# Optimization experiments

Hardware: AMD Instinct MI355X
Metric: run time of the kernel (lower is better)

## Reference

```python
import jax, jax.numpy as jnp
import numpy as np

D = 512      # d_model
H = 8        # n_heads
HD = D // H  # head_dim = 64
PS = 4       # patch_size
B, T, P = 4, 4096, 1024


def setup_inputs() -> dict:
    key = jax.random.key(0)
    ks = jax.random.split(key, 12)
    s = 1.0 / np.sqrt(D)
    return {
        "token_hidden": jax.random.normal(ks[0], (B, T, D), jnp.float32),
        "patch_hidden": jax.random.normal(ks[1], (B, P, D), jnp.float32),
        "Wq": jax.random.normal(ks[2], (D, D), jnp.float32) * s,
        "Wk": jax.random.normal(ks[3], (D, D), jnp.float32) * s,
        "Wv": jax.random.normal(ks[4], (D, D), jnp.float32) * s,
        "bq": jax.random.normal(ks[5], (D,), jnp.float32) * 0.02,
        "bk": jax.random.normal(ks[6], (D,), jnp.float32) * 0.02,
        "bv": jax.random.normal(ks[7], (D,), jnp.float32) * 0.02,
        "Wo": jax.random.normal(ks[8], (D, D), jnp.float32) * s,
        "bo": jax.random.normal(ks[9], (D,), jnp.float32) * 0.02,
    }


def reference(token_hidden, patch_hidden, Wq, Wk, Wv, bq, bk, bv, Wo, bo):
    b, t, _ = token_hidden.shape
    p = patch_hidden.shape[1]
    # QKV projections (equivalent to nn.MultiheadAttention in_proj)
    q = (token_hidden @ Wq + bq).reshape(b, t, H, HD)
    k = (patch_hidden @ Wk + bk).reshape(b, p, H, HD)
    v = (patch_hidden @ Wv + bv).reshape(b, p, H, HD)
    # scaled dot-product scores: [b, h, t, p]
    scores = jnp.einsum('bthd,bphd->bhtp', q, k) / jnp.sqrt(jnp.asarray(HD, q.dtype))
    # block-causal token-to-patch mask: token i attends to patches 0..i//PS
    allowed = jnp.arange(p)[None, :] <= (jnp.arange(t)[:, None] // PS)  # [t, p]
    scores = jnp.where(allowed[None, None, :, :], scores, -jnp.inf)
    attn = jax.nn.softmax(scores, axis=-1)
    ctx = jnp.einsum('bhtp,bphd->bthd', attn, v).reshape(b, t, D)
    out = ctx @ Wo + bo  # out_proj
    return token_hidden + out
```

## Files before the change

### kernel.cpp

```cpp
#include <hip/hip_runtime.h>
#include <stdint.h>

#define DM 512
#define NH 8
#define HDIM 64
#define TT 4096
#define PP 1024

typedef float f32x4 __attribute__((ext_vector_type(4)));
typedef __bf16 bf16x8 __attribute__((ext_vector_type(8)));
typedef __bf16 bf16x4 __attribute__((ext_vector_type(4)));
typedef unsigned short u16x8 __attribute__((ext_vector_type(8)));
typedef unsigned short u16x4 __attribute__((ext_vector_type(4)));
typedef unsigned int u32x2 __attribute__((ext_vector_type(2)));
typedef unsigned int u32x4 __attribute__((ext_vector_type(4)));

static __device__ __forceinline__ unsigned short f2bf(float f) {
  unsigned u = __builtin_bit_cast(unsigned, f);
  u += 0x7fff + ((u >> 16) & 1);
  return (unsigned short)(u >> 16);
}

static __device__ __forceinline__ unsigned packtr(float a, float b) {
  return __builtin_amdgcn_perm(__builtin_bit_cast(unsigned, b),
                               __builtin_bit_cast(unsigned, a), 0x07060302u);
}

static __device__ __forceinline__ float fexp2(float x) {
#if __has_builtin(__builtin_amdgcn_exp2f)
  return __builtin_amdgcn_exp2f(x);
#else
  return __expf(x * 0.69314718055994531f);
#endif
}

static __device__ __forceinline__ void load_lds16(const void* g, void* l) {
  __builtin_amdgcn_global_load_lds(
      (__attribute__((address_space(1))) void*)g,
      (__attribute__((address_space(3))) void*)l, 16, 0, 0);
}

static __device__ __forceinline__ f32x4 mfma16(bf16x8 a, bf16x8 b, f32x4 c) {
  return __builtin_amdgcn_mfma_f32_16x16x32_bf16(a, b, c, 0, 0, 0);
}

static __device__ __forceinline__ bf16x8 p_exchange(unsigned w0, unsigned w1,
                                                    unsigned w2, unsigned w3,
                                                    int q, int c) {
#if __has_builtin(__builtin_amdgcn_permlane32_swap) && \
    __has_builtin(__builtin_amdgcn_permlane16_swap)
  (void)q; (void)c;
  auto s02 = __builtin_amdgcn_permlane32_swap(w0, w2, false, false);
  auto t02 = __builtin_amdgcn_permlane16_swap(s02[0], s02[1], false, false);
  auto s13 = __builtin_amdgcn_permlane32_swap(w1, w3, false, false);
  auto t13 = __builtin_amdgcn_permlane16_swap(s13[0], s13[1], false, false);
  u32x4 pd = {(unsigned)t02[0], (unsigned)t13[0], (unsigned)t02[1], (unsigned)t13[1]};
  return __builtin_bit_cast(bf16x8, pd);
#else
  const int a0 = (c + (q & 1) * 32) * 4;
  const int a2 = (c + 16 + (q & 1) * 32) * 4;
  const bool lo = (q < 2);
  unsigned d0 = lo ? (unsigned)__builtin_amdgcn_ds_bpermute(a0, (int)w0)
                   : (unsigned)__builtin_amdgcn_ds_bpermute(a0, (int)w2);
  unsigned d1 = lo ? (unsigned)__builtin_amdgcn_ds_bpermute(a0, (int)w1)
                   : (unsigned)__builtin_amdgcn_ds_bpermute(a0, (int)w3);
  unsigned d2 = lo ? (unsigned)__builtin_amdgcn_ds_bpermute(a2, (int)w0)
                   : (unsigned)__builtin_amdgcn_ds_bpermute(a2, (int)w2);
  unsigned d3 = lo ? (unsigned)__builtin_amdgcn_ds_bpermute(a2, (int)w1)
                   : (unsigned)__builtin_amdgcn_ds_bpermute(a2, (int)w3);
  u32x4 pd = {d0, d1, d2, d3};
  return __builtin_bit_cast(bf16x8, pd);
#endif
}

static __device__ __forceinline__ int sw_rd(int c, int q) {
  return ((q + (c >> 1)) & 3) * 8;
}

__global__ __launch_bounds__(256) void k_convW(
    const float* __restrict__ wq, const float* __restrict__ wk,
    const float* __restrict__ wv, const float* __restrict__ wo,
    unsigned short* __restrict__ wt) {
  const int wi = blockIdx.x * 256 + threadIdx.x;
  int wid = wi >> 16;
  int e = (wi & 65535) << 2;
  int k = e >> 9, n = e & 511;
  const float* w = (wid == 0) ? wq : (wid == 1) ? wk : (wid == 2) ? wv : wo;
  f32x4 v = *(const f32x4*)&w[e];
  unsigned short* wtb = wt + (wid << 18);
#pragma unroll
  for (int i = 0; i < 4; ++i) wtb[(n + i) * 512 + k] = f2bf(v[i]);
}

template <int MODE>
__device__ __forceinline__ void gemm_qkv_body(
    const float* __restrict__ A, const unsigned short* __restrict__ Wt,
    const float* __restrict__ bias, unsigned short* __restrict__ outb,
    int bid, unsigned short* sA, unsigned short* sB, float scale) {
  const int tid = threadIdx.x;
  const int wave = tid >> 6, lane = tid & 63;
  const int q = lane >> 4, c = lane & 15;
  const int bm = bid >> 2, bn = bid & 3;
  const int wm = (wave >> 1) * 64, wn = (wave & 1) * 64;
  const int lr = lane >> 2, lc = (lane & 3) * 8;
  const int swW = (((lane & 3) + (lane >> 3)) & 3) * 8;
  const int swS = (((lane & 3) - (lane >> 3)) & 3) * 8;

  f32x4 acc[4][4];
#pragma unroll
  for (int i = 0; i < 4; ++i)
#pragma unroll
    for (int j = 0; j < 4; ++j) acc[i][j] = (f32x4){0.f, 0.f, 0.f, 0.f};

  const int rowA0 = bm * 128, rowB0 = bn * 128;

  f32x4 rA0[2][2], rA1[2][2];

  auto a_issue = [&](int t, f32x4 (&r)[2][2]) {
    const int kn = t * 32;
#pragma unroll
    for (int qq = 0; qq < 2; ++qq) {
      const float* src = &A[(rowA0 + (wave * 2 + qq) * 16 + lr) * 512 + kn + lc];
      r[qq][0] = *(const f32x4*)src;
      r[qq][1] = *(const f32x4*)(src + 4);
    }
  };
  auto a_write = [&](int t, f32x4 (&r)[2][2]) {
    unsigned short* dA = sA + (t & 1) * 4096;
#pragma unroll
    for (int qq = 0; qq < 2; ++qq) {
      u16x4 lo = __builtin_bit_cast(u16x4, __builtin_convertvector(r[qq][0], bf16x4));
      u16x4 hi = __builtin_bit_cast(u16x4, __builtin_convertvector(r[qq][1], bf16x4));
      u16x8 o = {lo[0], lo[1], lo[2], lo[3], hi[0], hi[1], hi[2], hi[3]};
      *(u16x8*)&dA[(wave * 2 + qq) * 512 + lr * 32 + swW] = o;
    }
  };
  auto b_issue = [&](int t) {
    const int kn = t * 32;
    unsigned short* dB = sB + (t % 3) * 4096;
#pragma unroll
    for (int qq = 0; qq < 2; ++qq) {
      const int chunk = wave * 2 + qq;
      load_lds16(&Wt[(rowB0 + chunk * 16 + lr) * 512 + kn + swS], &dB[chunk * 512]);
    }
  };

  a_issue(0, rA0);
  b_issue(0);
  a_issue(1, rA1);
  b_issue(1);
  asm volatile("s_waitcnt vmcnt(6)" ::: "memory");
  a_write(0, rA0);
  asm volatile("s_waitcnt lgkmcnt(0)" ::: "memory");
  __builtin_amdgcn_s_barrier();

#pragma unroll 1
  for (int i = 0; i < 16; ++i) {
    const bool ev = ((i & 1) == 0);
    if (i + 2 < 16) {
      if (ev) a_issue(i + 2, rA0);
      else    a_issue(i + 2, rA1);
      b_issue(i + 2);
    }
    const unsigned short* curA = sA + (i & 1) * 4096;
    const unsigned short* curB = sB + (i % 3) * 4096;
    bf16x8 af[4], bfr[4];
#pragma unroll
    for (int mt = 0; mt < 4; ++mt)
      af[mt] = __builtin_bit_cast(bf16x8,
          *(const u16x8*)&curA[(wm + mt * 16 + c) * 32 + sw_rd(c, q)]);
#pragma unroll
    for (int nt = 0; nt < 4; ++nt)
      bfr[nt] = __builtin_bit_cast(bf16x8,
          *(const u16x8*)&curB[(wn + nt * 16 + c) * 32 + sw_rd(c, q)]);
#pragma unroll
    for (int mt = 0; mt < 4; ++mt)
#pragma unroll
      for (int nt = 0; nt < 4; ++nt) {
        if (MODE == 2)
          acc[mt][nt] = mfma16(af[mt], bfr[nt], acc[mt][nt]);
        else
          acc[mt][nt] = mfma16(bfr[nt], af[mt], acc[mt][nt]);
      }
    if (i < 15) {
      if (i < 14) asm volatile("s_waitcnt vmcnt(6)" ::: "memory");
      else        asm volatile("s_waitcnt vmcnt(0)" ::: "memory");
      if (ev) a_write(i + 1, rA1);
      else    a_write(i + 1, rA0);
      asm volatile("s_waitcnt lgkmcnt(0)" ::: "memory");
      __builtin_amdgcn_s_barrier();
    }
  }

  if (MODE == 2) {
#pragma unroll
    for (int nt = 0; nt < 4; ++nt) {
      const int col = bn * 128 + wn + nt * 16 + c;
      const float bcol = bias[col];
#pragma unroll
      for (int mt = 0; mt < 4; ++mt) {
        const int row0 = bm * 128 + wm + mt * 16 + q * 4;
        u16x4 o;
#pragma unroll
        for (int r = 0; r < 4; ++r) o[r] = f2bf(acc[mt][nt][r] + bcol);
        *(u16x4*)&outb[((row0 >> 10) << 19) + (col << 10) + (row0 & 1023)] = o;
      }
    }
  } else {
#pragma unroll
    for (int mt = 0; mt < 4; ++mt) {
      const int row = bm * 128 + wm + mt * 16 + c;
#pragma unroll
      for (int nt = 0; nt < 4; ++nt) {
        const int col0 = bn * 128 + wn + nt * 16 + q * 4;
        const f32x4 bv = *(const f32x4*)&bias[col0];
        u16x4 o;
#pragma unroll
        for (int r = 0; r < 4; ++r) o[r] = f2bf((acc[mt][nt][r] + bv[r]) * scale);
        *(u16x4*)&outb[row * 512 + col0] = o;
      }
    }
  }
}

__global__ __launch_bounds__(256, 3) void k_gemm_qkv(
    const float* __restrict__ tok, const float* __restrict__ pat,
    const unsigned short* __restrict__ WT,
    const float* __restrict__ bq, const float* __restrict__ bk,
    const float* __restrict__ bv,
    unsigned short* __restrict__ QB, unsigned short* __restrict__ KB,
    unsigned short* __restrict__ VTB) {
  __shared__ unsigned short sA[2 * 128 * 32];
  __shared__ unsigned short sB[3 * 128 * 32];
  const int hw = blockIdx.x;
  const int bid = (hw & 7) * 96 + (hw >> 3);
  if (bid < 512) {
    gemm_qkv_body<0>(tok, WT, bq, QB, bid, sA, sB, 0.18033688011112042f);
  } else if (bid < 640) {
    gemm_qkv_body<1>(pat, WT + 262144, bk, KB, bid - 512, sA, sB, 1.0f);
  } else {
    gemm_qkv_body<2>(pat, WT + 524288, bv, VTB, bid - 640, sA, sB, 1.0f);
  }
}

__global__ __launch_bounds__(256) void k_gemm_o(
    const unsigned short* __restrict__ A, const unsigned short* __restrict__ Wt,
    const float* __restrict__ bias, float* __restrict__ outf,
    const float* __restrict__ resid) {
  __shared__ unsigned short sA[3 * 128 * 32];
  __shared__ unsigned short sB[3 * 128 * 32];
  const int tid = threadIdx.x;
  const int wave = tid >> 6, lane = tid & 63;
  const int q = lane >> 4, c = lane & 15;
  const int hw = blockIdx.x;
  const int obid = (hw & 7) * 64 + (hw >> 3);
  const int bm = obid >> 2, bn = obid & 3;
  const int wm = (wave >> 1) * 64, wn = (wave & 1) * 64;
  const int lr = lane >> 2;
  const int swS = (((lane & 3) - (lane >> 3)) & 3) * 8;

  f32x4 acc[4][4];
#pragma unroll
  for (int i = 0; i < 4; ++i)
#pragma unroll
    for (int j = 0; j < 4; ++j) acc[i][j] = (f32x4){0.f, 0.f, 0.f, 0.f};

  const int rowA0 = bm * 128, rowB0 = bn * 128;

  auto stage = [&](int t) {
    const int kn = t * 32;
    unsigned short* dA = sA + (t % 3) * 4096;
    unsigned short* dB = sB + (t % 3) * 4096;
#pragma unroll
    for (int qq = 0; qq < 2; ++qq) {
      const int chunk = wave * 2 + qq;
      load_lds16(&A[(rowA0 + chunk * 16 + lr) * 512 + kn + swS], &dA[chunk * 512]);
      load_lds16(&Wt[(rowB0 + chunk * 16 + lr) * 512 + kn + swS], &dB[chunk * 512]);
    }
  };

  stage(0);
  stage(1);
  asm volatile("s_waitcnt vmcnt(4)" ::: "memory");
  __builtin_amdgcn_s_barrier();

#pragma unroll 1
  for (int i = 0; i < 16; ++i) {
    if (i + 2 < 16) stage(i + 2);
    const unsigned short* curA = sA + (i % 3) * 4096;
    const unsigned short* curB = sB + (i % 3) * 4096;
    bf16x8 af[4], bfr[4];
#pragma unroll
    for (int mt = 0; mt < 4; ++mt)
      af[mt] = __builtin_bit_cast(bf16x8,
          *(const u16x8*)&curA[(wm + mt * 16 + c) * 32 + sw_rd(c, q)]);
#pragma unroll
    for (int nt = 0; nt < 4; ++nt)
      bfr[nt] = __builtin_bit_cast(bf16x8,
          *(const u16x8*)&curB[(wn + nt * 16 + c) * 32 + sw_rd(c, q)]);
#pragma unroll
    for (int mt = 0; mt < 4; ++mt)
#pragma unroll
      for (int nt = 0; nt < 4; ++nt)
        acc[mt][nt] = mfma16(bfr[nt], af[mt], acc[mt][nt]);
    if (i < 15) {
      if (i + 2 < 16) asm volatile("s_waitcnt vmcnt(4)" ::: "memory");
      else            asm volatile("s_waitcnt vmcnt(0)" ::: "memory");
      __builtin_amdgcn_s_barrier();
    }
  }

#pragma unroll
  for (int mt = 0; mt < 4; ++mt) {
    const int row = bm * 128 + wm + mt * 16 + c;
#pragma unroll
    for (int nt = 0; nt < 4; ++nt) {
      const int col0 = bn * 128 + wn + nt * 16 + q * 4;
      const int o = row * 512 + col0;
      const f32x4 bv = *(const f32x4*)&bias[col0];
      const f32x4 rv = *(const f32x4*)&resid[o];
      f32x4 ov;
#pragma unroll
      for (int r = 0; r < 4; ++r) ov[r] = acc[mt][nt][r] + bv[r] + rv[r];
      *(f32x4*)&outf[o] = ov;
    }
  }
}

__global__ __launch_bounds__(256) void k_attn(
    const unsigned short* __restrict__ Q,
    const unsigned short* __restrict__ K,
    const unsigned short* __restrict__ VT,
    unsigned short* __restrict__ CTX) {
  __shared__ unsigned short sK[2][32 * 88];
  __shared__ unsigned short sV[2][64 * 40];

  const int tid = threadIdx.x;
  const int lane = tid & 63;
  const int wave = tid >> 6;
  const int q = lane >> 4, c = lane & 15;

  const int g = blockIdx.x >> 5;
  const int tg = (g < 16) ? g : 47 - g;
  const int bh = blockIdx.x & 31;
  const int b = bh >> 3, h = bh & 7;
  const int t0 = tg * 128 + wave * 32;
  const int tA = t0 + c, tB = t0 + 16 + c;

  const int qbA = (b * TT + tA) * 512 + h * 64 + q * 8;
  const int qbB = (b * TT + tB) * 512 + h * 64 + q * 8;
  const bf16x8 qfA0 = __builtin_bit_cast(bf16x8, *(const u16x8*)&Q[qbA]);
  const bf16x8 qfA1 = __builtin_bit_cast(bf16x8, *(const u16x8*)&Q[qbA + 32]);
  const bf16x8 qfB0 = __builtin_bit_cast(bf16x8, *(const u16x8*)&Q[qbB]);
  const bf16x8 qfB1 = __builtin_bit_cast(bf16x8, *(const u16x8*)&Q[qbB + 32]);

  f32x4 oA[4], oB[4];
#pragma unroll
  for (int m = 0; m < 4; ++m) {
    oA[m] = (f32x4){0.f, 0.f, 0.f, 0.f};
    oB[m] = (f32x4){0.f, 0.f, 0.f, 0.f};
  }
  f32x4 lA = (f32x4){0.f, 0.f, 0.f, 0.f};
  f32x4 lB = lA;
  const u16x8 onesu = {0x3F80, 0x3F80, 0x3F80, 0x3F80, 0x3F80, 0x3F80, 0x3F80, 0x3F80};
  const bf16x8 ones = __builtin_bit_cast(bf16x8, onesu);

  const int ntile = tg + 1;
  const int krow = tid >> 3, kcol = (tid & 7) * 8;
  const int vrow = tid >> 2, vcol = (tid & 3) * 8;
  const int kg = (b * PP + krow) * 512 + h * 64 + kcol;
  const int vg = (b << 19) + ((h * 64 + vrow) << 10) + vcol;

  u16x8 kreg = *(const u16x8*)&K[kg];
  u16x8 vreg = *(const u16x8*)&VT[vg];
  *(u16x8*)&sK[0][krow * 88 + kcol] = kreg;
  *(u16x8*)&sV[0][vrow * 40 + vcol] = vreg;
  __syncthreads();

#pragma unroll 1
  for (int pt = 0; pt < ntile; ++pt) {
    const int buf = pt & 1;
    const bool more = (pt + 1 < ntile);
    if (more) {
      kreg = *(const u16x8*)&K[kg + (pt + 1) * 32 * 512];
      vreg = *(const u16x8*)&VT[vg + (pt + 1) * 32];
    }
    const unsigned short* bK = sK[buf];
    const unsigned short* bV = sV[buf];

    const bf16x8 ka0 = __builtin_bit_cast(bf16x8, *(const u16x8*)&bK[c * 88 + q * 8]);
    const bf16x8 ka1 = __builtin_bit_cast(bf16x8, *(const u16x8*)&bK[c * 88 + 32 + q * 8]);
    const bf16x8 kb0 = __builtin_bit_cast(bf16x8, *(const u16x8*)&bK[(16 + c) * 88 + q * 8]);
    const bf16x8 kb1 = __builtin_bit_cast(bf16x8, *(const u16x8*)&bK[(16 + c) * 88 + 32 + q * 8]);

    const f32x4 z = (f32x4){0.f, 0.f, 0.f, 0.f};
    __builtin_amdgcn_s_setprio(1);
    f32x4 sA0 = mfma16(ka1, qfA1, mfma16(ka0, qfA0, z));
    f32x4 sA1 = mfma16(kb1, qfA1, mfma16(kb0, qfA0, z));
    f32x4 sB0 = mfma16(ka1, qfB1, mfma16(ka0, qfB0, z));
    f32x4 sB1 = mfma16(kb1, qfB1, mfma16(kb0, qfB0, z));
    __builtin_amdgcn_s_setprio(0);

    if (pt + 1 == ntile) {
      const int p0 = pt * 32;
      const int limA = tA >> 2, limB = tB >> 2;
      const int pb0 = p0 + q * 4, pb1 = p0 + 16 + q * 4;
#pragma unroll
      for (int r = 0; r < 4; ++r) {
        if (pb0 + r > limA) sA0[r] = -1e30f;
        if (pb1 + r > limA) sA1[r] = -1e30f;
        if (pb0 + r > limB) sB0[r] = -1e30f;
        if (pb1 + r > limB) sB1[r] = -1e30f;
      }
    }

    float pA0[4], pA1[4], pB0[4], pB1[4];
#pragma unroll
    for (int r = 0; r < 4; ++r) {
      pA0[r] = fexp2(sA0[r]);
      pA1[r] = fexp2(sA1[r]);
      pB0[r] = fexp2(sB0[r]);
      pB1[r] = fexp2(sB1[r]);
    }

    const bf16x8 pbA = p_exchange(packtr(pA0[0], pA0[1]), packtr(pA0[2], pA0[3]),
                                  packtr(pA1[0], pA1[1]), packtr(pA1[2], pA1[3]), q, c);
    const bf16x8 pbB = p_exchange(packtr(pB0[0], pB0[1]), packtr(pB0[2], pB0[3]),
                                  packtr(pB1[0], pB1[1]), packtr(pB1[2], pB1[3]), q, c);

    __builtin_amdgcn_s_setprio(1);
#pragma unroll
    for (int mt = 0; mt < 4; ++mt) {
      const bf16x8 vf =
          __builtin_bit_cast(bf16x8, *(const u16x8*)&bV[(mt * 16 + c) * 40 + q * 8]);
      oA[mt] = mfma16(vf, pbA, oA[mt]);
      oB[mt] = mfma16(vf, pbB, oB[mt]);
    }
    lA = mfma16(ones, pbA, lA);
    lB = mfma16(ones, pbB, lB);
    __builtin_amdgcn_s_setprio(0);

    if (more) {
      *(u16x8*)&sK[buf ^ 1][krow * 88 + kcol] = kreg;
      *(u16x8*)&sV[buf ^ 1][vrow * 40 + vcol] = vreg;
      __syncthreads();
    }
  }

  const float invA = 1.f / lA[0];
  const float invB = 1.f / lB[0];
  const int obA = (b * TT + tA) * 512 + h * 64 + q * 4;
  const int obB = (b * TT + tB) * 512 + h * 64 + q * 4;
#pragma unroll
  for (int mt = 0; mt < 4; ++mt) {
    u16x4 oa, ob;
#pragma unroll
    for (int r = 0; r < 4; ++r) {
      oa[r] = f2bf(oA[mt][r] * invA);
      ob[r] = f2bf(oB[mt][r] * invB);
    }
    *(u16x4*)&CTX[obA + mt * 16] = oa;
    *(u16x4*)&CTX[obB + mt * 16] = ob;
  }
}

extern "C" void kernel_launch(void* const* d_in, const int* in_sizes, int n_in,
                              void* d_out, int out_size, void* d_ws, size_t ws_size,
                              hipStream_t stream) {
  const float* tok = (const float*)d_in[0];
  const float* pat = (const float*)d_in[1];
  const float* Wq = (const float*)d_in[2];
  const float* Wk = (const float*)d_in[3];
  const float* Wv = (const float*)d_in[4];
  const float* bq = (const float*)d_in[5];
  const float* bk = (const float*)d_in[6];
  const float* bv = (const float*)d_in[7];
  const float* Wo = (const float*)d_in[8];
  const float* bo = (const float*)d_in[9];
  float* out = (float*)d_out;

  unsigned short* ws = (unsigned short*)d_ws;
  unsigned short* WT = ws;
  unsigned short* QB = ws + 11534336;
  unsigned short* KB = ws + 19922944;
  unsigned short* VTB = ws + 22020096;
  unsigned short* CTX = ws + 24117248;

  k_convW<<<1024, 256, 0, stream>>>(Wq, Wk, Wv, Wo, WT);
  k_gemm_qkv<<<768, 256, 0, stream>>>(tok, pat, WT, bq, bk, bv, QB, KB, VTB);
  k_attn<<<1024, 256, 0, stream>>>(QB, KB, VTB, CTX);
  k_gemm_o<<<512, 256, 0, stream>>>(CTX, WT + 786432, bo, out, tok);
}
```

Before: 196.0 us.

## Double K-tile depth to 64 in projection GEMMs with 8-way LDS swizzle

```diff
diff --git a/kernel.cpp b/kernel.cpp
--- a/kernel.cpp
+++ b/kernel.cpp
@@ -73,9 +73,6 @@
 #endif
 }
 
-static __device__ __forceinline__ int sw_rd(int c, int q) {
-  return ((q + (c >> 1)) & 3) * 8;
-}
 
 __global__ __launch_bounds__(256) void k_convW(
     const float* __restrict__ wq, const float* __restrict__ wk,
@@ -102,9 +99,9 @@
   const int q = lane >> 4, c = lane & 15;
   const int bm = bid >> 2, bn = bid & 3;
   const int wm = (wave >> 1) * 64, wn = (wave & 1) * 64;
-  const int lr = lane >> 2, lc = (lane & 3) * 8;
-  const int swW = (((lane & 3) + (lane >> 3)) & 3) * 8;
-  const int swS = (((lane & 3) - (lane >> 3)) & 3) * 8;
+  const int ar = tid >> 1, ah = (tid & 1) * 32;
+  const int als = (tid & 1) * 4;
+  const int bg = (((lane & 7) - (lane >> 3)) & 7) * 8;
 
   f32x4 acc[4][4];
 #pragma unroll
@@ -114,80 +111,76 @@
 
   const int rowA0 = bm * 128, rowB0 = bn * 128;
 
-  f32x4 rA0[2][2], rA1[2][2];
-
-  auto a_issue = [&](int t, f32x4 (&r)[2][2]) {
-    const int kn = t * 32;
-#pragma unroll
-    for (int qq = 0; qq < 2; ++qq) {
-      const float* src = &A[(rowA0 + (wave * 2 + qq) * 16 + lr) * 512 + kn + lc];
-      r[qq][0] = *(const f32x4*)src;
-      r[qq][1] = *(const f32x4*)(src + 4);
-    }
+  f32x4 rA[8];
+
+  auto a_issue = [&](int t) {
+    const float* src = &A[(rowA0 + ar) * 512 + t * 64 + ah];
+#pragma unroll
+    for (int j = 0; j < 8; ++j) rA[j] = *(const f32x4*)(src + j * 4);
   };
-  auto a_write = [&](int t, f32x4 (&r)[2][2]) {
-    unsigned short* dA = sA + (t & 1) * 4096;
-#pragma unroll
-    for (int qq = 0; qq < 2; ++qq) {
-      u16x4 lo = __builtin_bit_cast(u16x4, __builtin_convertvector(r[qq][0], bf16x4));
-      u16x4 hi = __builtin_bit_cast(u16x4, __builtin_convertvector(r[qq][1], bf16x4));
+  auto a_write = [&](int t) {
+    unsigned short* dA = sA + (t & 1) * 8192;
+#pragma unroll
+    for (int j = 0; j < 4; ++j) {
+      u16x4 lo = __builtin_bit_cast(u16x4, __builtin_convertvector(rA[2 * j], bf16x4));
+      u16x4 hi = __builtin_bit_cast(u16x4, __builtin_convertvector(rA[2 * j + 1], bf16x4));
       u16x8 o = {lo[0], lo[1], lo[2], lo[3], hi[0], hi[1], hi[2], hi[3]};
-      *(u16x8*)&dA[(wave * 2 + qq) * 512 + lr * 32 + swW] = o;
+      const int phys = ((als + j) + (ar & 7)) & 7;
+      *(u16x8*)&dA[ar * 64 + phys * 8] = o;
     }
   };
   auto b_issue = [&](int t) {
-    const int kn = t * 32;
-    unsigned short* dB = sB + (t % 3) * 4096;
-#pragma unroll
-    for (int qq = 0; qq < 2; ++qq) {
-      const int chunk = wave * 2 + qq;
-      load_lds16(&Wt[(rowB0 + chunk * 16 + lr) * 512 + kn + swS], &dB[chunk * 512]);
+    unsigned short* dB = sB + (t & 1) * 8192;
+#pragma unroll
+    for (int ch = 0; ch < 4; ++ch) {
+      const int r0 = wave * 32 + ch * 8;
+      load_lds16(&Wt[(rowB0 + r0 + (lane >> 3)) * 512 + t * 64 + bg],
+                 &dB[r0 * 64]);
     }
   };
 
-  a_issue(0, rA0);
+  a_issue(0);
   b_issue(0);
-  a_issue(1, rA1);
-  b_issue(1);
-  asm volatile("s_waitcnt vmcnt(6)" ::: "memory");
-  a_write(0, rA0);
-  asm volatile("s_waitcnt lgkmcnt(0)" ::: "memory");
+  asm volatile("s_waitcnt vmcnt(4)" ::: "memory");
+  a_write(0);
+  asm volatile("s_waitcnt vmcnt(0) lgkmcnt(0)" ::: "memory");
   __builtin_amdgcn_s_barrier();
 
 #pragma unroll 1
-  for (int i = 0; i < 16; ++i) {
-    const bool ev = ((i & 1) == 0);
-    if (i + 2 < 16) {
-      if (ev) a_issue(i + 2, rA0);
-      else    a_issue(i + 2, rA1);
-      b_issue(i + 2);
-    }
-    const unsigned short* curA = sA + (i & 1) * 4096;
-    const unsigned short* curB = sB + (i % 3) * 4096;
-    bf16x8 af[4], bfr[4];
-#pragma unroll
-    for (int mt = 0; mt < 4; ++mt)
-      af[mt] = __builtin_bit_cast(bf16x8,
-          *(const u16x8*)&curA[(wm + mt * 16 + c) * 32 + sw_rd(c, q)]);
-#pragma unroll
-    for (int nt = 0; nt < 4; ++nt)
-      bfr[nt] = __builtin_bit_cast(bf16x8,
-          *(const u16x8*)&curB[(wn + nt * 16 + c) * 32 + sw_rd(c, q)]);
-#pragma unroll
-    for (int mt = 0; mt < 4; ++mt)
-#pragma unroll
-      for (int nt = 0; nt < 4; ++nt) {
-        if (MODE == 2)
-          acc[mt][nt] = mfma16(af[mt], bfr[nt], acc[mt][nt]);
-        else
-          acc[mt][nt] = mfma16(bfr[nt], af[mt], acc[mt][nt]);
-      }
-    if (i < 15) {
-      if (i < 14) asm volatile("s_waitcnt vmcnt(6)" ::: "memory");
-      else        asm volatile("s_waitcnt vmcnt(0)" ::: "memory");
-      if (ev) a_write(i + 1, rA1);
-      else    a_write(i + 1, rA0);
-      asm volatile("s_waitcnt lgkmcnt(0)" ::: "memory");
+  for (int i = 0; i < 8; ++i) {
+    const bool more = (i + 1 < 8);
+    if (more) {
+      a_issue(i + 1);
+      b_issue(i + 1);
+    }
+    const unsigned short* curA = sA + (i & 1) * 8192;
+    const unsigned short* curB = sB + (i & 1) * 8192;
+#pragma unroll
+    for (int ks = 0; ks < 2; ++ks) {
+      const int ph = ((ks * 4 + q + (c & 7)) & 7) * 8;
+      bf16x8 af[4], bfr[4];
+#pragma unroll
+      for (int mt = 0; mt < 4; ++mt)
+        af[mt] = __builtin_bit_cast(bf16x8,
+            *(const u16x8*)&curA[(wm + mt * 16 + c) * 64 + ph]);
+#pragma unroll
+      for (int nt = 0; nt < 4; ++nt)
+        bfr[nt] = __builtin_bit_cast(bf16x8,
+            *(const u16x8*)&curB[(wn + nt * 16 + c) * 64 + ph]);
+#pragma unroll
+      for (int mt = 0; mt < 4; ++mt)
+#pragma unroll
+        for (int nt = 0; nt < 4; ++nt) {
+          if (MODE == 2)
+            acc[mt][nt] = mfma16(af[mt], bfr[nt], acc[mt][nt]);
+          else
+            acc[mt][nt] = mfma16(bfr[nt], af[mt], acc[mt][nt]);
+        }
+    }
+    if (more) {
+      asm volatile("s_waitcnt vmcnt(4)" ::: "memory");
+      a_write(i + 1);
+      asm volatile("s_waitcnt vmcnt(0) lgkmcnt(0)" ::: "memory");
       __builtin_amdgcn_s_barrier();
     }
   }
@@ -223,15 +216,15 @@
   }
 }
 
-__global__ __launch_bounds__(256, 3) void k_gemm_qkv(
+__global__ __launch_bounds__(256, 2) void k_gemm_qkv(
     const float* __restrict__ tok, const float* __restrict__ pat,
     const unsigned short* __restrict__ WT,
     const float* __restrict__ bq, const float* __restrict__ bk,
     const float* __restrict__ bv,
     unsigned short* __restrict__ QB, unsigned short* __restrict__ KB,
     unsigned short* __restrict__ VTB) {
-  __shared__ unsigned short sA[2 * 128 * 32];
-  __shared__ unsigned short sB[3 * 128 * 32];
+  __shared__ unsigned short sA[2 * 128 * 64];
+  __shared__ unsigned short sB[2 * 128 * 64];
   const int hw = blockIdx.x;
   const int bid = (hw & 7) * 96 + (hw >> 3);
   if (bid < 512) {
@@ -243,12 +236,12 @@
   }
 }
 
-__global__ __launch_bounds__(256) void k_gemm_o(
+__global__ __launch_bounds__(256, 2) void k_gemm_o(
     const unsigned short* __restrict__ A, const unsigned short* __restrict__ Wt,
     const float* __restrict__ bias, float* __restrict__ outf,
     const float* __restrict__ resid) {
-  __shared__ unsigned short sA[3 * 128 * 32];
-  __shared__ unsigned short sB[3 * 128 * 32];
+  __shared__ unsigned short sA[2 * 128 * 64];
+  __shared__ unsigned short sB[2 * 128 * 64];
   const int tid = threadIdx.x;
   const int wave = tid >> 6, lane = tid & 63;
   const int q = lane >> 4, c = lane & 15;
@@ -256,8 +249,7 @@
   const int obid = (hw & 7) * 64 + (hw >> 3);
   const int bm = obid >> 2, bn = obid & 3;
   const int wm = (wave >> 1) * 64, wn = (wave & 1) * 64;
-  const int lr = lane >> 2;
-  const int swS = (((lane & 3) - (lane >> 3)) & 3) * 8;
+  const int bg = (((lane & 7) - (lane >> 3)) & 7) * 8;
 
   f32x4 acc[4][4];
 #pragma unroll
@@ -268,44 +260,47 @@
   const int rowA0 = bm * 128, rowB0 = bn * 128;
 
   auto stage = [&](int t) {
-    const int kn = t * 32;
-    unsigned short* dA = sA + (t % 3) * 4096;
-    unsigned short* dB = sB + (t % 3) * 4096;
-#pragma unroll
-    for (int qq = 0; qq < 2; ++qq) {
-      const int chunk = wave * 2 + qq;
-      load_lds16(&A[(rowA0 + chunk * 16 + lr) * 512 + kn + swS], &dA[chunk * 512]);
-      load_lds16(&Wt[(rowB0 + chunk * 16 + lr) * 512 + kn + swS], &dB[chunk * 512]);
+    unsigned short* dA = sA + (t & 1) * 8192;
+    unsigned short* dB = sB + (t & 1) * 8192;
+#pragma unroll
+    for (int ch = 0; ch < 4; ++ch) {
+      const int r0 = wave * 32 + ch * 8;
+      const int rsrc = r0 + (lane >> 3);
+      load_lds16(&A[(rowA0 + rsrc) * 512 + t * 64 + bg], &dA[r0 * 64]);
+      load_lds16(&Wt[(rowB0 + rsrc) * 512 + t * 64 + bg], &dB[r0 * 64]);
     }
   };
 
   stage(0);
-  stage(1);
-  asm volatile("s_waitcnt vmcnt(4)" ::: "memory");
+  asm volatile("s_waitcnt vmcnt(0)" ::: "memory");
   __builtin_amdgcn_s_barrier();
 
 #pragma unroll 1
-  for (int i = 0; i < 16; ++i) {
-    if (i + 2 < 16) stage(i + 2);
-    const unsigned short* curA = sA + (i % 3) * 4096;
-    const unsigned short* curB = sB + (i % 3) * 4096;
-    bf16x8 af[4], bfr[4];
-#pragma unroll
-    for (int mt = 0; mt < 4; ++mt)
-      af[mt] = __builtin_bit_cast(bf16x8,
-          *(const u16x8*)&curA[(wm + mt * 16 + c) * 32 + sw_rd(c, q)]);
-#pragma unroll
-    for (int nt = 0; nt < 4; ++nt)
-      bfr[nt] = __builtin_bit_cast(bf16x8,
-          *(const u16x8*)&curB[(wn + nt * 16 + c) * 32 + sw_rd(c, q)]);
-#pragma unroll
-    for (int mt = 0; mt < 4; ++mt)
+  for (int i = 0; i < 8; ++i) {
+    const bool more = (i + 1 < 8);
+    if (more) stage(i + 1);
+    const unsigned short* curA = sA + (i & 1) * 8192;
+    const unsigned short* curB = sB + (i & 1) * 8192;
+#pragma unroll
+    for (int ks = 0; ks < 2; ++ks) {
+      const int ph = ((ks * 4 + q + (c & 7)) & 7) * 8;
+      bf16x8 af[4], bfr[4];
+#pragma unroll
+      for (int mt = 0; mt < 4; ++mt)
+        af[mt] = __builtin_bit_cast(bf16x8,
+            *(const u16x8*)&curA[(wm + mt * 16 + c) * 64 + ph]);
 #pragma unroll
       for (int nt = 0; nt < 4; ++nt)
-        acc[mt][nt] = mfma16(bfr[nt], af[mt], acc[mt][nt]);
-    if (i < 15) {
-      if (i + 2 < 16) asm volatile("s_waitcnt vmcnt(4)" ::: "memory");
-      else            asm volatile("s_waitcnt vmcnt(0)" ::: "memory");
+        bfr[nt] = __builtin_bit_cast(bf16x8,
+            *(const u16x8*)&curB[(wn + nt * 16 + c) * 64 + ph]);
+#pragma unroll
+      for (int mt = 0; mt < 4; ++mt)
+#pragma unroll
+        for (int nt = 0; nt < 4; ++nt)
+          acc[mt][nt] = mfma16(bfr[nt], af[mt], acc[mt][nt]);
+    }
+    if (more) {
+      asm volatile("s_waitcnt vmcnt(0)" ::: "memory");
       __builtin_amdgcn_s_barrier();
     }
   }
```

Result: slower. 205.0 us (+4.6%).

## Load GEMM A operand directly into MFMA registers, bypassing LDS staging

Applied to the files above, without the earlier changes.

```diff
diff --git a/kernel.cpp b/kernel.cpp
--- a/kernel.cpp
+++ b/kernel.cpp
@@ -96,14 +96,13 @@
 __device__ __forceinline__ void gemm_qkv_body(
     const float* __restrict__ A, const unsigned short* __restrict__ Wt,
     const float* __restrict__ bias, unsigned short* __restrict__ outb,
-    int bid, unsigned short* sA, unsigned short* sB, float scale) {
+    int bid, unsigned short* sB, float scale) {
   const int tid = threadIdx.x;
   const int wave = tid >> 6, lane = tid & 63;
   const int q = lane >> 4, c = lane & 15;
   const int bm = bid >> 2, bn = bid & 3;
   const int wm = (wave >> 1) * 64, wn = (wave & 1) * 64;
-  const int lr = lane >> 2, lc = (lane & 3) * 8;
-  const int swW = (((lane & 3) + (lane >> 3)) & 3) * 8;
+  const int lr = lane >> 2;
   const int swS = (((lane & 3) - (lane >> 3)) & 3) * 8;
 
   f32x4 acc[4][4];
@@ -113,62 +112,36 @@
     for (int j = 0; j < 4; ++j) acc[i][j] = (f32x4){0.f, 0.f, 0.f, 0.f};
 
   const int rowA0 = bm * 128, rowB0 = bn * 128;
-
-  f32x4 rA0[2][2], rA1[2][2];
-
-  auto a_issue = [&](int t, f32x4 (&r)[2][2]) {
-    const int kn = t * 32;
-#pragma unroll
-    for (int qq = 0; qq < 2; ++qq) {
-      const float* src = &A[(rowA0 + (wave * 2 + qq) * 16 + lr) * 512 + kn + lc];
-      r[qq][0] = *(const f32x4*)src;
-      r[qq][1] = *(const f32x4*)(src + 4);
-    }
-  };
-  auto a_write = [&](int t, f32x4 (&r)[2][2]) {
-    unsigned short* dA = sA + (t & 1) * 4096;
-#pragma unroll
-    for (int qq = 0; qq < 2; ++qq) {
-      u16x4 lo = __builtin_bit_cast(u16x4, __builtin_convertvector(r[qq][0], bf16x4));
-      u16x4 hi = __builtin_bit_cast(u16x4, __builtin_convertvector(r[qq][1], bf16x4));
-      u16x8 o = {lo[0], lo[1], lo[2], lo[3], hi[0], hi[1], hi[2], hi[3]};
-      *(u16x8*)&dA[(wave * 2 + qq) * 512 + lr * 32 + swW] = o;
+  const float* aBase = &A[(rowA0 + wm + c) * 512 + q * 8];
+
+  f32x4 rE[4][2], rO[4][2];
+
+  auto a_issue = [&](int t, f32x4 (&r)[4][2]) {
+#pragma unroll
+    for (int mt = 0; mt < 4; ++mt) {
+      const float* p = aBase + mt * 16 * 512 + t * 32;
+      r[mt][0] = *(const f32x4*)p;
+      r[mt][1] = *(const f32x4*)(p + 4);
     }
   };
   auto b_issue = [&](int t) {
-    const int kn = t * 32;
     unsigned short* dB = sB + (t % 3) * 4096;
 #pragma unroll
     for (int qq = 0; qq < 2; ++qq) {
       const int chunk = wave * 2 + qq;
-      load_lds16(&Wt[(rowB0 + chunk * 16 + lr) * 512 + kn + swS], &dB[chunk * 512]);
-    }
-  };
-
-  a_issue(0, rA0);
-  b_issue(0);
-  a_issue(1, rA1);
-  b_issue(1);
-  asm volatile("s_waitcnt vmcnt(6)" ::: "memory");
-  a_write(0, rA0);
-  asm volatile("s_waitcnt lgkmcnt(0)" ::: "memory");
-  __builtin_amdgcn_s_barrier();
-
-#pragma unroll 1
-  for (int i = 0; i < 16; ++i) {
-    const bool ev = ((i & 1) == 0);
-    if (i + 2 < 16) {
-      if (ev) a_issue(i + 2, rA0);
-      else    a_issue(i + 2, rA1);
-      b_issue(i + 2);
-    }
-    const unsigned short* curA = sA + (i & 1) * 4096;
+      load_lds16(&Wt[(rowB0 + chunk * 16 + lr) * 512 + t * 32 + swS],
+                 &dB[chunk * 512]);
+    }
+  };
+  auto compute = [&](int i, f32x4 (&r)[4][2]) {
     const unsigned short* curB = sB + (i % 3) * 4096;
     bf16x8 af[4], bfr[4];
 #pragma unroll
-    for (int mt = 0; mt < 4; ++mt)
-      af[mt] = __builtin_bit_cast(bf16x8,
-          *(const u16x8*)&curA[(wm + mt * 16 + c) * 32 + sw_rd(c, q)]);
+    for (int mt = 0; mt < 4; ++mt) {
+      bf16x4 lo = __builtin_convertvector(r[mt][0], bf16x4);
+      bf16x4 hi = __builtin_convertvector(r[mt][1], bf16x4);
+      af[mt] = (bf16x8){lo[0], lo[1], lo[2], lo[3], hi[0], hi[1], hi[2], hi[3]};
+    }
 #pragma unroll
     for (int nt = 0; nt < 4; ++nt)
       bfr[nt] = __builtin_bit_cast(bf16x8,
@@ -182,12 +155,30 @@
         else
           acc[mt][nt] = mfma16(bfr[nt], af[mt], acc[mt][nt]);
       }
-    if (i < 15) {
-      if (i < 14) asm volatile("s_waitcnt vmcnt(6)" ::: "memory");
-      else        asm volatile("s_waitcnt vmcnt(0)" ::: "memory");
-      if (ev) a_write(i + 1, rA1);
-      else    a_write(i + 1, rA0);
-      asm volatile("s_waitcnt lgkmcnt(0)" ::: "memory");
+  };
+
+  b_issue(0);
+  b_issue(1);
+  a_issue(0, rE);
+  asm volatile("s_waitcnt vmcnt(10)" ::: "memory");
+  __builtin_amdgcn_s_barrier();
+
+#pragma unroll 1
+  for (int ii = 0; ii < 8; ++ii) {
+    const int i0 = 2 * ii;
+    if (i0 + 2 < 16) b_issue(i0 + 2);
+    a_issue(i0 + 1, rO);
+    compute(i0, rE);
+    if (i0 < 14) asm volatile("s_waitcnt vmcnt(10)" ::: "memory");
+    else         asm volatile("s_waitcnt vmcnt(8)" ::: "memory");
+    __builtin_amdgcn_s_barrier();
+    const int i1 = i0 + 1;
+    if (i1 + 2 < 16) b_issue(i1 + 2);
+    if (i1 + 1 < 16) a_issue(i1 + 1, rE);
+    compute(i1, rO);
+    if (i1 < 15) {
+      if (i1 < 14) asm volatile("s_waitcnt vmcnt(10)" ::: "memory");
+      else         asm volatile("s_waitcnt vmcnt(8)" ::: "memory");
       __builtin_amdgcn_s_barrier();
     }
   }
@@ -230,24 +221,22 @@
     const float* __restrict__ bv,
     unsigned short* __restrict__ QB, unsigned short* __restrict__ KB,
     unsigned short* __restrict__ VTB) {
-  __shared__ unsigned short sA[2 * 128 * 32];
   __shared__ unsigned short sB[3 * 128 * 32];
   const int hw = blockIdx.x;
   const int bid = (hw & 7) * 96 + (hw >> 3);
   if (bid < 512) {
-    gemm_qkv_body<0>(tok, WT, bq, QB, bid, sA, sB, 0.18033688011112042f);
+    gemm_qkv_body<0>(tok, WT, bq, QB, bid, sB, 0.18033688011112042f);
   } else if (bid < 640) {
-    gemm_qkv_body<1>(pat, WT + 262144, bk, KB, bid - 512, sA, sB, 1.0f);
+    gemm_qkv_body<1>(pat, WT + 262144, bk, KB, bid - 512, sB, 1.0f);
   } else {
-    gemm_qkv_body<2>(pat, WT + 524288, bv, VTB, bid - 640, sA, sB, 1.0f);
-  }
-}
-
-__global__ __launch_bounds__(256) void k_gemm_o(
+    gemm_qkv_body<2>(pat, WT + 524288, bv, VTB, bid - 640, sB, 1.0f);
+  }
+}
+
+__global__ __launch_bounds__(256, 2) void k_gemm_o(
     const unsigned short* __restrict__ A, const unsigned short* __restrict__ Wt,
     const float* __restrict__ bias, float* __restrict__ outf,
     const float* __restrict__ resid) {
-  __shared__ unsigned short sA[3 * 128 * 32];
   __shared__ unsigned short sB[3 * 128 * 32];
   const int tid = threadIdx.x;
   const int wave = tid >> 6, lane = tid & 63;
@@ -266,34 +255,27 @@
     for (int j = 0; j < 4; ++j) acc[i][j] = (f32x4){0.f, 0.f, 0.f, 0.f};
 
   const int rowA0 = bm * 128, rowB0 = bn * 128;
-
-  auto stage = [&](int t) {
-    const int kn = t * 32;
-    unsigned short* dA = sA + (t % 3) * 4096;
+  const unsigned short* aBase = &A[(rowA0 + wm + c) * 512 + q * 8];
+
+  u16x8 rE[4], rO[4];
+
+  auto a_issue = [&](int t, u16x8 (&r)[4]) {
+#pragma unroll
+    for (int mt = 0; mt < 4; ++mt)
+      r[mt] = *(const u16x8*)(aBase + mt * 16 * 512 + t * 32);
+  };
+  auto b_issue = [&](int t) {
     unsigned short* dB = sB + (t % 3) * 4096;
 #pragma unroll
     for (int qq = 0; qq < 2; ++qq) {
       const int chunk = wave * 2 + qq;
-      load_lds16(&A[(rowA0 + chunk * 16 + lr) * 512 + kn + swS], &dA[chunk * 512]);
-      load_lds16(&Wt[(rowB0 + chunk * 16 + lr) * 512 + kn + swS], &dB[chunk * 512]);
-    }
-  };
-
-  stage(0);
-  stage(1);
-  asm volatile("s_waitcnt vmcnt(4)" ::: "memory");
-  __builtin_amdgcn_s_barrier();
-
-#pragma unroll 1
-  for (int i = 0; i < 16; ++i) {
-    if (i + 2 < 16) stage(i + 2);
-    const unsigned short* curA = sA + (i % 3) * 4096;
+      load_lds16(&Wt[(rowB0 + chunk * 16 + lr) * 512 + t * 32 + swS],
+                 &dB[chunk * 512]);
+    }
+  };
+  auto compute = [&](int i, u16x8 (&r)[4]) {
     const unsigned short* curB = sB + (i % 3) * 4096;
-    bf16x8 af[4], bfr[4];
-#pragma unroll
-    for (int mt = 0; mt < 4; ++mt)
-      af[mt] = __builtin_bit_cast(bf16x8,
-          *(const u16x8*)&curA[(wm + mt * 16 + c) * 32 + sw_rd(c, q)]);
+    bf16x8 bfr[4];
 #pragma unroll
     for (int nt = 0; nt < 4; ++nt)
       bfr[nt] = __builtin_bit_cast(bf16x8,
@@ -302,10 +284,32 @@
     for (int mt = 0; mt < 4; ++mt)
 #pragma unroll
       for (int nt = 0; nt < 4; ++nt)
-        acc[mt][nt] = mfma16(bfr[nt], af[mt], acc[mt][nt]);
-    if (i < 15) {
-      if (i + 2 < 16) asm volatile("s_waitcnt vmcnt(4)" ::: "memory");
-      else            asm volatile("s_waitcnt vmcnt(0)" ::: "memory");
+        acc[mt][nt] = mfma16(bfr[nt], __builtin_bit_cast(bf16x8, r[mt]),
+                             acc[mt][nt]);
+  };
+
+  b_issue(0);
+  b_issue(1);
+  a_issue(0, rE);
+  asm volatile("s_waitcnt vmcnt(6)" ::: "memory");
+  __builtin_amdgcn_s_barrier();
+
+#pragma unroll 1
+  for (int ii = 0; ii < 8; ++ii) {
+    const int i0 = 2 * ii;
+    if (i0 + 2 < 16) b_issue(i0 + 2);
+    a_issue(i0 + 1, rO);
+    compute(i0, rE);
+    if (i0 < 14) asm volatile("s_waitcnt vmcnt(6)" ::: "memory");
+    else         asm volatile("s_waitcnt vmcnt(4)" ::: "memory");
+    __builtin_amdgcn_s_barrier();
+    const int i1 = i0 + 1;
+    if (i1 + 2 < 16) b_issue(i1 + 2);
+    if (i1 + 1 < 16) a_issue(i1 + 1, rE);
+    compute(i1, rO);
+    if (i1 < 15) {
+      if (i1 < 14) asm volatile("s_waitcnt vmcnt(6)" ::: "memory");
+      else         asm volatile("s_waitcnt vmcnt(4)" ::: "memory");
       __builtin_amdgcn_s_barrier();
     }
   }
```

New measurement: 225.9 us. 1.15x slower.
